# Optimization experiments

Hardware: AMD Instinct MI355X
Metric: run time of the kernel (lower is better)

The kernel has to match this reference:

```python
import jax, jax.numpy as jnp
import numpy as np

# ---- module hyperparameters (init_kwargs) ----
M = 6          # truncation level
D = 5          # path dimension
C = 4.0        # phi parameter
A = 1.0        # phi parameter a
SIGLEN = (D ** (M + 1) - 1) // (D - 1) - 1  # 19530
B, S = 64, 32  # batch x samples
N_BISECT = 100

# level id (1..M) of each signature coordinate: d^k coords at level k
LEVELS = jnp.asarray(np.repeat(np.arange(1, M + 1), [D ** k for k in range(1, M + 1)]), dtype=jnp.float32)  # [L]
# one-hot [L, M] mapping coordinates to their level, for per-level squared-norm sums
LEVEL_ONEHOT = jnp.asarray((np.repeat(np.arange(1, M + 1), [D ** k for k in range(1, M + 1)])[:, None] == np.arange(1, M + 1)[None, :]).astype(np.float32))


def setup_inputs() -> dict:
    key = jax.random.key(0)
    signatures = jax.random.normal(key, (B, S, SIGLEN), dtype=jnp.float32) * 0.5
    return {"signatures": signatures}


def _phi(x):
    # phi(x) = x for x <= C, else C + C^(1+a) (C^-a - x^-a)/a
    return jnp.where(x > C, C + C ** (1.0 + A) * (C ** (-A) - x ** (-A)) / A, x)


def _dilatation_norm(x):
    """x: [B,S,L] signatures. Returns norm lambda in [0,1], shape [B,S,1].
    Solves c0 + sum_k c_k t^{2k} = 0 on [0,2] by bisection (replaces brentq)."""
    x2 = x * x
    norm_quad = 1.0 + jnp.sum(x2, axis=-1)          # [B,S]
    c0 = 1.0 - _phi(norm_quad)                      # [B,S], <= 0
    ck = jnp.einsum('bsl,lm->bsm', x2, LEVEL_ONEHOT)  # [B,S,M] per-level squared norms
    coeffs = jnp.concatenate([c0[..., None], ck], axis=-1)  # [B,S,M+1]
    ks = jnp.arange(M + 1, dtype=jnp.float32)

    def poly(t):  # t: [B,S]
        return jnp.sum(coeffs * (t[..., None] ** 2) ** ks, axis=-1)

    def body(i, carry):
        lo, hi = carry
        mid = 0.5 * (lo + hi)
        neg = poly(mid) < 0.0
        return jnp.where(neg, mid, lo), jnp.where(neg, hi, mid)

    lo = jnp.zeros_like(c0)
    hi = jnp.full_like(c0, 2.0)
    lo, hi = jax.lax.fori_loop(0, N_BISECT, body, (lo, hi))
    root = 0.5 * (lo + hi)
    root = jnp.where(jnp.all(jnp.isfinite(coeffs), axis=-1), root, 0.0)
    root = jnp.minimum(root, 1.0)  # clamp as in dilatation()
    return root[..., None]          # [B,S,1]


def reference(signatures):
    # Normalization.apply + rescale + mean over samples (martingale_indices=None path)
    norm = _dilatation_norm(signatures)                       # [B,S,1]
    scaled = signatures * norm ** LEVELS[None, None, :]       # [B,S,L]
    return jnp.mean(scaled, axis=-2)                          # [B,L]
```

## Files before the change

kernel.cpp:

```cpp
#include <hip/hip_runtime.h>
#include <math.h>

#define BATCH   64
#define SAMP    32
#define SIGLEN  19530
#define NROWS   (BATCH * SAMP)
#define NF2     (SIGLEN / 2)
#define NBISECT 40
#define CHB     39


__device__ float g_pw[NROWS * 6];

__device__ __forceinline__ int level0(int l) {
    return (l >= 5) + (l >= 30) + (l >= 155) + (l >= 780) + (l >= 3905);
}

__global__ __launch_bounds__(256) void es_phase1_kernel(const float* __restrict__ x) {
    const int r = blockIdx.x;
    const int t = threadIdx.x;
    const float* __restrict__ row = x + (size_t)r * SIGLEN;

    float a1 = 0.f, a2 = 0.f, a3 = 0.f, a4 = 0.f, a5 = 0.f, a6 = 0.f;

    if (t < 5)            { float v = row[t]; a1 += v * v; }
    else if (t < 30)      { float v = row[t]; a2 += v * v; }
    else if (t < 155)     { float v = row[t]; a3 += v * v; }
    for (int l = 155 + t; l < 780; l += 256) { float v = row[l]; a4 += v * v; }

    const int head = (r & 1) ? 2 : 0;
    if (head) { if (t == 0)  { float v0 = row[780],   v1 = row[781];   a5 += v0*v0 + v1*v1; } }
    else      { if (t == 32) { float v0 = row[19528], v1 = row[19529]; a6 += v0*v0 + v1*v1; } }

    const float4* __restrict__ p4 = (const float4*)(row + 780 + head);
    const int lb = 780 + head;
    #pragma unroll 4
    for (int q = t; q < 4687; q += 256) {
        const float4 v = p4[q];
        const int l = lb + 4 * q;
        const float s = v.x*v.x + v.y*v.y + v.z*v.z + v.w*v.w;
        if (l >= 3905)      a6 += s;
        else if (l <= 3901) a5 += s;
        else {
            ((l     >= 3905) ? a6 : a5) += v.x * v.x;
            ((l + 1 >= 3905) ? a6 : a5) += v.y * v.y;
            ((l + 2 >= 3905) ? a6 : a5) += v.z * v.z;
            ((l + 3 >= 3905) ? a6 : a5) += v.w * v.w;
        }
    }

    #pragma unroll
    for (int off = 32; off > 0; off >>= 1) {
        a1 += __shfl_xor(a1, off); a2 += __shfl_xor(a2, off);
        a3 += __shfl_xor(a3, off); a4 += __shfl_xor(a4, off);
        a5 += __shfl_xor(a5, off); a6 += __shfl_xor(a6, off);
    }
    __shared__ float red[4][6];
    const int wave = t >> 6, lane = t & 63;
    if (lane == 0) {
        red[wave][0] = a1; red[wave][1] = a2; red[wave][2] = a3;
        red[wave][3] = a4; red[wave][4] = a5; red[wave][5] = a6;
    }
    __syncthreads();

    if (t == 0) {
        float s1 = 0.f, s2 = 0.f, s3 = 0.f, s4 = 0.f, s5 = 0.f, s6 = 0.f;
        #pragma unroll
        for (int w = 0; w < 4; ++w) {
            s1 += red[w][0]; s2 += red[w][1]; s3 += red[w][2];
            s4 += red[w][3]; s5 += red[w][4]; s6 += red[w][5];
        }
        const float total = s1 + s2 + s3 + s4 + s5 + s6;
        const float nq  = 1.0f + total;
        const float phi = (nq > 4.0f) ? (8.0f - 16.0f / nq) : nq;
        const float c0  = 1.0f - phi;
        const bool  fin = isfinite(c0) && isfinite(total);

        float lo = 0.0f, hi = 2.0f;
        #pragma unroll 4
        for (int i = 0; i < NBISECT; ++i) {
            const float mid = 0.5f * (lo + hi);
            const float u = mid * mid;
            const float pv = ((((((s6*u + s5)*u + s4)*u + s3)*u + s2)*u + s1)*u) + c0;
            const bool neg = pv < 0.0f;
            lo = neg ? mid : lo;
            hi = neg ? hi : mid;
        }
        float root = 0.5f * (lo + hi);
        if (!fin) root = 0.0f;
        root = fminf(root, 1.0f);

        const float inv = 1.0f / SAMP;
        float w1 = root, w2 = w1*root, w3 = w2*root, w4 = w3*root, w5 = w4*root, w6 = w5*root;
        float* dst = g_pw + (size_t)r * 6;
        dst[0] = w1 * inv; dst[1] = w2 * inv; dst[2] = w3 * inv;
        dst[3] = w4 * inv; dst[4] = w5 * inv; dst[5] = w6 * inv;
    }
}

__global__ __launch_bounds__(256) void es_phase2_kernel(const float* __restrict__ x,
                                                        float* __restrict__ out) {
    const int b = blockIdx.y;
    const int t = threadIdx.x;

    __shared__ float wsh[SAMP * 6];
    if (t < SAMP * 6) wsh[t] = g_pw[(size_t)b * (SAMP * 6) + t];
    __syncthreads();

    const int j = blockIdx.x * 256 + t;
    if (j >= NF2) return;

    const int l0 = 2 * j;
    const int levA = level0(l0);
    const int levB = level0(l0 + 1);

    const float2* __restrict__ x2p = (const float2*)x;
    const unsigned base = (unsigned)b * (SAMP * NF2) + (unsigned)j;

    float acc0 = 0.f, acc1 = 0.f;
    if (levA == levB) {
        #pragma unroll
        for (int s = 0; s < SAMP; ++s) {
            const float  ws = wsh[s * 6 + levA];
            const float2 v  = x2p[base + (unsigned)s * NF2];
            acc0 += v.x * ws;
            acc1 += v.y * ws;
        }
    } else {
        #pragma unroll
        for (int s = 0; s < SAMP; ++s) {
            const float2 v = x2p[base + (unsigned)s * NF2];
            acc0 += v.x * wsh[s * 6 + levA];
            acc1 += v.y * wsh[s * 6 + levB];
        }
    }

    float2 rv; rv.x = acc0; rv.y = acc1;
    ((float2*)out)[(unsigned)b * NF2 + (unsigned)j] = rv;
}

extern "C" void kernel_launch(void* const* d_in, const int* in_sizes, int n_in,
                              void* d_out, int out_size, void* d_ws, size_t ws_size,
                              hipStream_t stream) {
    const float* x = (const float*)d_in[0];
    float* out = (float*)d_out;
    (void)d_ws; (void)ws_size;

    es_phase1_kernel<<<NROWS, 256, 0, stream>>>(x);
    dim3 gridB(CHB, BATCH);
    es_phase2_kernel<<<gridB, 256, 0, stream>>>(x, out);
}
```

Before: 255.0 us.

## Widen phase-2 per-thread work to eight columns with 128-bit aligned loads

The weighted-mean phase now gives each thread eight consecutive signature coordinates instead of two. It uses float4/float2 vector loads that follow the row parity, since rows of odd length alternate their 16-byte alignment. The block size drops to 64 threads, so the grid still has 39x64 blocks. The aim is fewer, wider memory transactions and more loads in flight per thread. In exchange each wave has fewer lanes per block, total parallelism is lower, and lanes now access memory with a 32-byte stride.

```diff
diff --git a/kernel.cpp b/kernel.cpp
--- a/kernel.cpp
+++ b/kernel.cpp
@@ -5,9 +5,10 @@
 #define SAMP    32
 #define SIGLEN  19530
 #define NROWS   (BATCH * SAMP)
-#define NF2     (SIGLEN / 2)
 #define NBISECT 40
-#define CHB     39
+#define PER_T   8
+#define TPR     2442
+#define GX      39
 
 
 __device__ float g_pw[NROWS * 6];
@@ -98,45 +99,75 @@
     }
 }
 
-__global__ __launch_bounds__(256) void es_phase2_kernel(const float* __restrict__ x,
-                                                        float* __restrict__ out) {
+__global__ __launch_bounds__(64) void es_phase2_kernel(const float* __restrict__ x,
+                                                       float* __restrict__ out) {
     const int b = blockIdx.y;
     const int t = threadIdx.x;
 
     __shared__ float wsh[SAMP * 6];
-    if (t < SAMP * 6) wsh[t] = g_pw[(size_t)b * (SAMP * 6) + t];
+    for (int i = t; i < SAMP * 6; i += 64)
+        wsh[i] = g_pw[(size_t)b * (SAMP * 6) + i];
     __syncthreads();
 
-    const int j = blockIdx.x * 256 + t;
-    if (j >= NF2) return;
+    const int idx = blockIdx.x * 64 + t;
+    if (idx >= TPR) return;
+    const int l0 = idx * PER_T;
+    const int ncol = min(PER_T, SIGLEN - l0);
 
-    const int l0 = 2 * j;
-    const int levA = level0(l0);
-    const int levB = level0(l0 + 1);
+    int lev[PER_T];
+    #pragma unroll
+    for (int c = 0; c < PER_T; ++c) lev[c] = level0(min(l0 + c, SIGLEN - 1));
+    const bool uni = (lev[0] == lev[PER_T - 1]) & (ncol == PER_T);
 
-    const float2* __restrict__ x2p = (const float2*)x;
-    const unsigned base = (unsigned)b * (SAMP * NF2) + (unsigned)j;
+    float acc[PER_T];
+    #pragma unroll
+    for (int c = 0; c < PER_T; ++c) acc[c] = 0.f;
 
-    float acc0 = 0.f, acc1 = 0.f;
-    if (levA == levB) {
-        #pragma unroll
+    const float* __restrict__ xb = x + (size_t)b * (SAMP * (size_t)SIGLEN) + l0;
+
+    if (uni) {
+        const int lv = lev[0];
+        #pragma unroll 8
         for (int s = 0; s < SAMP; ++s) {
-            const float  ws = wsh[s * 6 + levA];
-            const float2 v  = x2p[base + (unsigned)s * NF2];
-            acc0 += v.x * ws;
-            acc1 += v.y * ws;
+            const float ws = wsh[s * 6 + lv];
+            const float* rp = xb + (size_t)s * SIGLEN;
+            float v0, v1, v2, v3, v4, v5, v6, v7;
+            if ((s & 1) == 0) {
+                const float4 qa = *(const float4*)rp;
+                const float4 qb = *(const float4*)(rp + 4);
+                v0 = qa.x; v1 = qa.y; v2 = qa.z; v3 = qa.w;
+                v4 = qb.x; v5 = qb.y; v6 = qb.z; v7 = qb.w;
+            } else {
+                const float2 h  = *(const float2*)rp;
+                const float4 m  = *(const float4*)(rp + 2);
+                const float2 tl = *(const float2*)(rp + 6);
+                v0 = h.x;  v1 = h.y;  v2 = m.x;  v3 = m.y;
+                v4 = m.z;  v5 = m.w;  v6 = tl.x; v7 = tl.y;
+            }
+            acc[0] += v0 * ws; acc[1] += v1 * ws; acc[2] += v2 * ws; acc[3] += v3 * ws;
+            acc[4] += v4 * ws; acc[5] += v5 * ws; acc[6] += v6 * ws; acc[7] += v7 * ws;
         }
     } else {
-        #pragma unroll
         for (int s = 0; s < SAMP; ++s) {
-            const float2 v = x2p[base + (unsigned)s * NF2];
-            acc0 += v.x * wsh[s * 6 + levA];
-            acc1 += v.y * wsh[s * 6 + levB];
+            const float* rp = xb + (size_t)s * SIGLEN;
+            for (int c = 0; c < ncol; ++c)
+                acc[c] += rp[c] * wsh[s * 6 + lev[c]];
         }
     }
 
-    float2 rv; rv.x = acc0; rv.y = acc1;
-    ((float2*)out)[(unsigned)b * NF2 + (unsigned)j] = rv;
+    float* op = out + (size_t)b * SIGLEN + l0;
+    if (ncol == PER_T) {
+        if ((b & 1) == 0) {
+            *(float4*)op       = make_float4(acc[0], acc[1], acc[2], acc[3]);
+            *(float4*)(op + 4) = make_float4(acc[4], acc[5], acc[6], acc[7]);
+        } else {
+            *(float2*)op       = make_float2(acc[0], acc[1]);
+            *(float4*)(op + 2) = make_float4(acc[2], acc[3], acc[4], acc[5]);
+            *(float2*)(op + 6) = make_float2(acc[6], acc[7]);
+        }
+    } else {
+        for (int c = 0; c < ncol; ++c) op[c] = acc[c];
+    }
 }
 
 extern "C" void kernel_launch(void* const* d_in, const int* in_sizes, int n_in,
@@ -147,6 +178,6 @@
     (void)d_ws; (void)ws_size;
 
     es_phase1_kernel<<<NROWS, 256, 0, stream>>>(x);
-    dim3 gridB(CHB, BATCH);
-    es_phase2_kernel<<<gridB, 256, 0, stream>>>(x, out);
+    dim3 gridB(GX, BATCH);
+    es_phase2_kernel<<<gridB, 64, 0, stream>>>(x, out);
 }
```

Result: slower. 286.8 us (+12.5%).

## Widen phase-2 loads to float4 with even/odd row alignment and cross-thread fixup

Applied to the files above, without the earlier changes.

Phase 2 now gives each thread four output columns instead of two. Each thread issues 16-byte loads: even sample rows read at col and odd rows at col+2, because the odd row length SIGLEN breaks 16-byte alignment on alternate rows. Partial sums for odd rows are shifted to the neighbouring thread with shuffles and shared memory, and a separate scalar path handles the final partial chunk. The aim is fewer, wider memory transactions in the bandwidth-bound reduction, at the cost of extra shuffles, a block barrier and more complex indexing.

```diff
diff --git a/kernel.cpp b/kernel.cpp
--- a/kernel.cpp
+++ b/kernel.cpp
@@ -5,9 +5,9 @@
 #define SAMP    32
 #define SIGLEN  19530
 #define NROWS   (BATCH * SAMP)
-#define NF2     (SIGLEN / 2)
 #define NBISECT 40
-#define CHB     39
+#define P2COLS  1024
+#define P2GX    20
 
 
 __device__ float g_pw[NROWS * 6];
@@ -100,43 +100,97 @@
 
 __global__ __launch_bounds__(256) void es_phase2_kernel(const float* __restrict__ x,
                                                         float* __restrict__ out) {
-    const int b = blockIdx.y;
-    const int t = threadIdx.x;
+    const int b  = blockIdx.y;
+    const int k  = blockIdx.x;
+    const int t  = threadIdx.x;
+    const int c0 = k * P2COLS;
 
     __shared__ float wsh[SAMP * 6];
+    __shared__ float xw[3][2];
     if (t < SAMP * 6) wsh[t] = g_pw[(size_t)b * (SAMP * 6) + t];
     __syncthreads();
 
-    const int j = blockIdx.x * 256 + t;
-    if (j >= NF2) return;
-
-    const int l0 = 2 * j;
-    const int levA = level0(l0);
-    const int levB = level0(l0 + 1);
-
-    const float2* __restrict__ x2p = (const float2*)x;
-    const unsigned base = (unsigned)b * (SAMP * NF2) + (unsigned)j;
-
-    float acc0 = 0.f, acc1 = 0.f;
-    if (levA == levB) {
+    const float* __restrict__ xb = x + (size_t)b * (SAMP * (size_t)SIGLEN);
+
+    if (c0 + P2COLS > SIGLEN) {
+        const int col = c0 + t;
+        if (col < SIGLEN) {
+            const int lv = level0(col);
+            float acc = 0.f;
+            #pragma unroll 8
+            for (int s = 0; s < SAMP; ++s)
+                acc += xb[(size_t)s * SIGLEN + col] * wsh[s * 6 + lv];
+            out[(size_t)b * SIGLEN + col] = acc;
+        }
+        return;
+    }
+
+    const int col = c0 + 4 * t;
+    float ae0=0.f, ae1=0.f, ae2=0.f, ae3=0.f;
+    float ao0=0.f, ao1=0.f, ao2=0.f, ao3=0.f;
+    float ah0=0.f, ah1=0.f;
+
+    const float* __restrict__ pe = xb + col;
+    const float* __restrict__ po = xb + col + 2;
+
+    const int lA = level0(col), lB = level0(col + 5);
+    if (lA == lB) {
         #pragma unroll
-        for (int s = 0; s < SAMP; ++s) {
-            const float  ws = wsh[s * 6 + levA];
-            const float2 v  = x2p[base + (unsigned)s * NF2];
-            acc0 += v.x * ws;
-            acc1 += v.y * ws;
+        for (int sp = 0; sp < 16; ++sp) {
+            const int se = 2 * sp, so = 2 * sp + 1;
+            const float4 ve = *(const float4*)(pe + (size_t)se * SIGLEN);
+            const float4 vo = *(const float4*)(po + (size_t)so * SIGLEN);
+            const float we = wsh[se * 6 + lA];
+            const float wo = wsh[so * 6 + lA];
+            ae0 += ve.x * we; ae1 += ve.y * we; ae2 += ve.z * we; ae3 += ve.w * we;
+            ao0 += vo.x * wo; ao1 += vo.y * wo; ao2 += vo.z * wo; ao3 += vo.w * wo;
         }
     } else {
+        const int le0 = level0(col),     le1 = level0(col + 1);
+        const int le2 = level0(col + 2), le3 = level0(col + 3);
+        const int lo2 = level0(col + 4), lo3 = level0(col + 5);
+        #pragma unroll 4
+        for (int sp = 0; sp < 16; ++sp) {
+            const int se = 2 * sp, so = 2 * sp + 1;
+            const float4 ve = *(const float4*)(pe + (size_t)se * SIGLEN);
+            const float4 vo = *(const float4*)(po + (size_t)so * SIGLEN);
+            ae0 += ve.x * wsh[se*6 + le0]; ae1 += ve.y * wsh[se*6 + le1];
+            ae2 += ve.z * wsh[se*6 + le2]; ae3 += ve.w * wsh[se*6 + le3];
+            ao0 += vo.x * wsh[so*6 + le2]; ao1 += vo.y * wsh[so*6 + le3];
+            ao2 += vo.z * wsh[so*6 + lo2]; ao3 += vo.w * wsh[so*6 + lo3];
+        }
+    }
+
+    if (t == 0) {
+        const int lh0 = level0(c0), lh1 = level0(c0 + 1);
         #pragma unroll
-        for (int s = 0; s < SAMP; ++s) {
-            const float2 v = x2p[base + (unsigned)s * NF2];
-            acc0 += v.x * wsh[s * 6 + levA];
-            acc1 += v.y * wsh[s * 6 + levB];
-        }
-    }
-
-    float2 rv; rv.x = acc0; rv.y = acc1;
-    ((float2*)out)[(unsigned)b * NF2 + (unsigned)j] = rv;
+        for (int so = 1; so < SAMP; so += 2) {
+            const float2 vh = *(const float2*)(xb + (size_t)so * SIGLEN + c0);
+            ah0 += vh.x * wsh[so * 6 + lh0];
+            ah1 += vh.y * wsh[so * 6 + lh1];
+        }
+    }
+
+    float po2 = __shfl_up(ao2, 1);
+    float po3 = __shfl_up(ao3, 1);
+    const int wave = t >> 6, lane = t & 63;
+    if (lane == 63 && wave < 3) { xw[wave][0] = ao2; xw[wave][1] = ao3; }
+    __syncthreads();
+    if (lane == 0) {
+        if (wave > 0) { po2 = xw[wave - 1][0]; po3 = xw[wave - 1][1]; }
+        else          { po2 = ah0;             po3 = ah1;             }
+    }
+
+    const float f0 = ae0 + po2, f1 = ae1 + po3;
+    const float f2 = ae2 + ao0, f3 = ae3 + ao1;
+
+    float* op = out + (size_t)b * SIGLEN + col;
+    if ((b & 1) == 0) {
+        *(float4*)op = make_float4(f0, f1, f2, f3);
+    } else {
+        *(float2*)op       = make_float2(f0, f1);
+        *(float2*)(op + 2) = make_float2(f2, f3);
+    }
 }
 
 extern "C" void kernel_launch(void* const* d_in, const int* in_sizes, int n_in,
@@ -147,6 +201,6 @@
     (void)d_ws; (void)ws_size;
 
     es_phase1_kernel<<<NROWS, 256, 0, stream>>>(x);
-    dim3 gridB(CHB, BATCH);
+    dim3 gridB(P2GX, BATCH);
     es_phase2_kernel<<<gridB, 256, 0, stream>>>(x, out);
 }
```

Result: no change. 251.4 us (-1.4%).

## Fuse norm and weighted mean into one pass with register-held rows and atomics

Applied to the files above, without the earlier changes.

Merges the two kernels into one. Each block keeps its whole signature row in registers, computes the bisection root, then atomically adds the weighted values into the zeroed output, so the input is read from HBM once instead of twice. Blocks are remapped so that each batch's samples are spread across the grid, and the loads are nontemporal. In exchange the kernel issues about 40M float atomics, needs a memset, and carries heavy register pressure. The summation order is also no longer deterministic.

```diff
diff --git a/kernel.cpp b/kernel.cpp
--- a/kernel.cpp
+++ b/kernel.cpp
@@ -5,49 +5,75 @@
 #define SAMP    32
 #define SIGLEN  19530
 #define NROWS   (BATCH * SAMP)
-#define NF2     (SIGLEN / 2)
 #define NBISECT 40
-#define CHB     39
 
 
-__device__ float g_pw[NROWS * 6];
+typedef float f32x4 __attribute__((ext_vector_type(4)));
 
-__device__ __forceinline__ int level0(int l) {
-    return (l >= 5) + (l >= 30) + (l >= 155) + (l >= 780) + (l >= 3905);
-}
-
-__global__ __launch_bounds__(256) void es_phase1_kernel(const float* __restrict__ x) {
-    const int r = blockIdx.x;
-    const int t = threadIdx.x;
+__global__ __launch_bounds__(256, 4) void es_onepass_kernel(
+        const float* __restrict__ x, float* __restrict__ out) {
+    const int blk = blockIdx.x;
+    const int m   = blk & 7;
+    const int h   = blk >> 3;
+    const int bat = m * 8 + (h >> 5);
+    const int s   = h & 31;
+    const int r   = bat * SAMP + s;
+    const int t   = threadIdx.x;
     const float* __restrict__ row = x + (size_t)r * SIGLEN;
 
     float a1 = 0.f, a2 = 0.f, a3 = 0.f, a4 = 0.f, a5 = 0.f, a6 = 0.f;
 
-    if (t < 5)            { float v = row[t]; a1 += v * v; }
-    else if (t < 30)      { float v = row[t]; a2 += v * v; }
-    else if (t < 155)     { float v = row[t]; a3 += v * v; }
-    for (int l = 155 + t; l < 780; l += 256) { float v = row[l]; a4 += v * v; }
+    float eT = 0.f;
+    if (t < 155) {
+        eT = row[t];
+        const float v = eT * eT;
+        if (t < 5) a1 += v; else if (t < 30) a2 += v; else a3 += v;
+    }
+    float e1 = row[155 + t]; a4 += e1 * e1;
+    float e2 = row[411 + t]; a4 += e2 * e2;
+    float e3 = 0.f;
+    if (t < 113) { e3 = row[667 + t]; a4 += e3 * e3; }
 
     const int head = (r & 1) ? 2 : 0;
-    if (head) { if (t == 0)  { float v0 = row[780],   v1 = row[781];   a5 += v0*v0 + v1*v1; } }
-    else      { if (t == 32) { float v0 = row[19528], v1 = row[19529]; a6 += v0*v0 + v1*v1; } }
+    float sp0 = 0.f, sp1 = 0.f;
+    float sq0 = 0.f, sq1 = 0.f, sq2 = 0.f, sq3 = 0.f;
+    if (head) {
+        if (t == 0)  { sp0 = row[780];  sp1 = row[781];
+                       a5 += sp0*sp0 + sp1*sp1; }
+        if (t == 64) { sq0 = row[3902]; sq1 = row[3903]; sq2 = row[3904]; sq3 = row[3905];
+                       a5 += sq0*sq0 + sq1*sq1 + sq2*sq2; a6 += sq3*sq3; }
+    } else {
+        if (t == 0)  { sp0 = row[19528]; sp1 = row[19529];
+                       a6 += sp0*sp0 + sp1*sp1; }
+        if (t == 64) { sq0 = row[3904]; sq1 = row[3905]; sq2 = row[3906]; sq3 = row[3907];
+                       a5 += sq0*sq0; a6 += sq1*sq1 + sq2*sq2 + sq3*sq3; }
+    }
 
-    const float4* __restrict__ p4 = (const float4*)(row + 780 + head);
-    const int lb = 780 + head;
-    #pragma unroll 4
-    for (int q = t; q < 4687; q += 256) {
-        const float4 v = p4[q];
-        const int l = lb + 4 * q;
-        const float s = v.x*v.x + v.y*v.y + v.z*v.z + v.w*v.w;
-        if (l >= 3905)      a6 += s;
-        else if (l <= 3901) a5 += s;
-        else {
-            ((l     >= 3905) ? a6 : a5) += v.x * v.x;
-            ((l + 1 >= 3905) ? a6 : a5) += v.y * v.y;
-            ((l + 2 >= 3905) ? a6 : a5) += v.z * v.z;
-            ((l + 3 >= 3905) ? a6 : a5) += v.w * v.w;
-        }
-    }
+    const int cA = 780 + head;
+    const int cB = head ? 3906 : 3908;
+    const int Q5 = head ? 780  : 781;
+    const int Q6 = head ? 3906 : 3905;
+    const f32x4* __restrict__ pA = (const f32x4*)(row + cA);
+    const f32x4* __restrict__ pB = (const f32x4*)(row + cB);
+
+    f32x4 va0, va1, va2, va3 = {0.f, 0.f, 0.f, 0.f};
+#define DOT4(v) ((v).x*(v).x + (v).y*(v).y + (v).z*(v).z + (v).w*(v).w)
+    va0 = __builtin_nontemporal_load(pA + t);        a5 += DOT4(va0);
+    va1 = __builtin_nontemporal_load(pA + t + 256);  a5 += DOT4(va1);
+    va2 = __builtin_nontemporal_load(pA + t + 512);  a5 += DOT4(va2);
+    const bool vA3 = (t + 768) < Q5;
+    if (vA3) { va3 = __builtin_nontemporal_load(pA + t + 768); a5 += DOT4(va3); }
+
+    f32x4 vb0,vb1,vb2,vb3,vb4,vb5,vb6,vb7,vb8,vb9,vb10,vb11,vb12,vb13,vb14;
+    f32x4 vb15 = {0.f, 0.f, 0.f, 0.f};
+#define LOADB(k) { vb##k = __builtin_nontemporal_load(pB + t + 256*(k)); a6 += DOT4(vb##k); }
+    LOADB(0)  LOADB(1)  LOADB(2)  LOADB(3)  LOADB(4)
+    LOADB(5)  LOADB(6)  LOADB(7)  LOADB(8)  LOADB(9)
+    LOADB(10) LOADB(11) LOADB(12) LOADB(13) LOADB(14)
+#undef LOADB
+    const bool vB15 = (t + 3840) < Q6;
+    if (vB15) { vb15 = __builtin_nontemporal_load(pB + t + 3840); a6 += DOT4(vb15); }
+#undef DOT4
 
     #pragma unroll
     for (int off = 32; off > 0; off >>= 1) {
@@ -56,6 +82,7 @@
         a5 += __shfl_xor(a5, off); a6 += __shfl_xor(a6, off);
     }
     __shared__ float red[4][6];
+    __shared__ float wlds[6];
     const int wave = t >> 6, lane = t & 63;
     if (lane == 0) {
         red[wave][0] = a1; red[wave][1] = a2; red[wave][2] = a3;
@@ -92,51 +119,56 @@
 
         const float inv = 1.0f / SAMP;
         float w1 = root, w2 = w1*root, w3 = w2*root, w4 = w3*root, w5 = w4*root, w6 = w5*root;
-        float* dst = g_pw + (size_t)r * 6;
-        dst[0] = w1 * inv; dst[1] = w2 * inv; dst[2] = w3 * inv;
-        dst[3] = w4 * inv; dst[4] = w5 * inv; dst[5] = w6 * inv;
+        wlds[0] = w1 * inv; wlds[1] = w2 * inv; wlds[2] = w3 * inv;
+        wlds[3] = w4 * inv; wlds[4] = w5 * inv; wlds[5] = w6 * inv;
     }
-}
-
-__global__ __launch_bounds__(256) void es_phase2_kernel(const float* __restrict__ x,
-                                                        float* __restrict__ out) {
-    const int b = blockIdx.y;
-    const int t = threadIdx.x;
-
-    __shared__ float wsh[SAMP * 6];
-    if (t < SAMP * 6) wsh[t] = g_pw[(size_t)b * (SAMP * 6) + t];
     __syncthreads();
 
-    const int j = blockIdx.x * 256 + t;
-    if (j >= NF2) return;
+    const float w4f = wlds[3], w5f = wlds[4], w6f = wlds[5];
+    float* __restrict__ ob = out + (size_t)bat * SIGLEN;
 
-    const int l0 = 2 * j;
-    const int levA = level0(l0);
-    const int levB = level0(l0 + 1);
+    if (t < 155) {
+        const float wE = (t < 5) ? wlds[0] : ((t < 30) ? wlds[1] : wlds[2]);
+        unsafeAtomicAdd(&ob[t], eT * wE);
+    }
+    unsafeAtomicAdd(&ob[155 + t], e1 * w4f);
+    unsafeAtomicAdd(&ob[411 + t], e2 * w4f);
+    if (t < 113) unsafeAtomicAdd(&ob[667 + t], e3 * w4f);
 
-    const float2* __restrict__ x2p = (const float2*)x;
-    const unsigned base = (unsigned)b * (SAMP * NF2) + (unsigned)j;
-
-    float acc0 = 0.f, acc1 = 0.f;
-    if (levA == levB) {
-        #pragma unroll
-        for (int s = 0; s < SAMP; ++s) {
-            const float  ws = wsh[s * 6 + levA];
-            const float2 v  = x2p[base + (unsigned)s * NF2];
-            acc0 += v.x * ws;
-            acc1 += v.y * ws;
-        }
+    if (head) {
+        if (t == 0)  { unsafeAtomicAdd(&ob[780],  sp0 * w5f);
+                       unsafeAtomicAdd(&ob[781],  sp1 * w5f); }
+        if (t == 64) { unsafeAtomicAdd(&ob[3902], sq0 * w5f);
+                       unsafeAtomicAdd(&ob[3903], sq1 * w5f);
+                       unsafeAtomicAdd(&ob[3904], sq2 * w5f);
+                       unsafeAtomicAdd(&ob[3905], sq3 * w6f); }
     } else {
-        #pragma unroll
-        for (int s = 0; s < SAMP; ++s) {
-            const float2 v = x2p[base + (unsigned)s * NF2];
-            acc0 += v.x * wsh[s * 6 + levA];
-            acc1 += v.y * wsh[s * 6 + levB];
-        }
+        if (t == 0)  { unsafeAtomicAdd(&ob[19528], sp0 * w6f);
+                       unsafeAtomicAdd(&ob[19529], sp1 * w6f); }
+        if (t == 64) { unsafeAtomicAdd(&ob[3904], sq0 * w5f);
+                       unsafeAtomicAdd(&ob[3905], sq1 * w6f);
+                       unsafeAtomicAdd(&ob[3906], sq2 * w6f);
+                       unsafeAtomicAdd(&ob[3907], sq3 * w6f); }
     }
 
-    float2 rv; rv.x = acc0; rv.y = acc1;
-    ((float2*)out)[(unsigned)b * NF2 + (unsigned)j] = rv;
+#define ATOM4(base, v, wf) { \
+        unsafeAtomicAdd(&ob[(base) + 0], (v).x * (wf)); \
+        unsafeAtomicAdd(&ob[(base) + 1], (v).y * (wf)); \
+        unsafeAtomicAdd(&ob[(base) + 2], (v).z * (wf)); \
+        unsafeAtomicAdd(&ob[(base) + 3], (v).w * (wf)); }
+
+    ATOM4(cA + 4*t,          va0, w5f)
+    ATOM4(cA + 4*(t + 256),  va1, w5f)
+    ATOM4(cA + 4*(t + 512),  va2, w5f)
+    if (vA3) ATOM4(cA + 4*(t + 768), va3, w5f)
+
+#define ATOMB(k) ATOM4(cB + 4*(t + 256*(k)), vb##k, w6f)
+    ATOMB(0)  ATOMB(1)  ATOMB(2)  ATOMB(3)  ATOMB(4)
+    ATOMB(5)  ATOMB(6)  ATOMB(7)  ATOMB(8)  ATOMB(9)
+    ATOMB(10) ATOMB(11) ATOMB(12) ATOMB(13) ATOMB(14)
+    if (vB15) ATOMB(15)
+#undef ATOMB
+#undef ATOM4
 }
 
 extern "C" void kernel_launch(void* const* d_in, const int* in_sizes, int n_in,
@@ -146,7 +178,6 @@
     float* out = (float*)d_out;
     (void)d_ws; (void)ws_size;
 
-    es_phase1_kernel<<<NROWS, 256, 0, stream>>>(x);
-    dim3 gridB(CHB, BATCH);
-    es_phase2_kernel<<<gridB, 256, 0, stream>>>(x, out);
+    hipMemsetAsync(out, 0, (size_t)out_size, stream);
+    es_onepass_kernel<<<NROWS, 256, 0, stream>>>(x, out);
 }
```

Result: slower. 752.0 us (+194.9%).
